# Performance work log

Hardware: AMD Instinct MI355X
Metric: run time of the kernel (lower is better)

The kernel has to match this reference:

```python
import jax, jax.numpy as jnp
import numpy as np

B, L, D, H = 1, 1024, 768, 12
h = D // H  # 64
EPS = 1e-5
ALPHA = 0.01  # leaky relu slope


def setup_inputs() -> dict:
    key = jax.random.key(0)
    ks = jax.random.split(key, 10)
    s = 0.02
    f32 = jnp.float32
    return {
        "x": jax.random.normal(ks[0], (B, L, D), f32),
        "filters": jax.random.normal(ks[1], (L, h), f32) * s,  # spectral filters [L, h]
        "wq_w": jax.random.normal(ks[2], (D, D), f32) * s,
        "wq_b": jnp.zeros((D,), f32),
        "wk_w": jax.random.normal(ks[3], (D, D), f32) * s,
        "wk_b": jnp.zeros((D,), f32),
        "wv_w": jax.random.normal(ks[4], (D, D), f32) * s,
        "wv_b": jnp.zeros((D,), f32),
        "wo_w": jax.random.normal(ks[5], (D, D), f32) * s,
        "wo_b": jnp.zeros((D,), f32),
        "wg_w": jax.random.normal(ks[6], (h * h, 1), f32) * s,
        "wg_b": jnp.zeros((1,), f32),
        "qk_scale": jnp.ones((1, H, 1), f32) + jax.random.normal(ks[7], (1, H, 1), f32) * 0.02,
        "kv_scale": jnp.ones((1, H, 1, 1, 1), f32) + jax.random.normal(ks[8], (1, H, 1, 1, 1), f32) * 0.02,
    }


def _causal_fft_conv(f, u):
    """Per-head-channel causal FFT convolution. f: [L,h], u: [B,H,L,h] -> [B,H,L,h]."""
    n = 2 * L  # >= L + L - 1 for linear (full) convolution
    Ff = jnp.fft.rfft(f, n=n, axis=0)            # [n//2+1, h]
    Uf = jnp.fft.rfft(u, n=n, axis=2)            # [B,H,n//2+1,h]
    y = jnp.fft.irfft(Uf * Ff[None, None], n=n, axis=2)
    return y[:, :, :L, :]


def _l2norm(t):
    # matches F.normalize(dim=-1): x / max(||x||, 1e-12)
    nrm = jnp.sqrt(jnp.sum(t * t, axis=-1, keepdims=True))
    return t / jnp.maximum(nrm, 1e-12)


def _combine(a, b):
    """Associative combine: (m, s, n, Z, g) running-max / exp-sum / exp-weighted-v / outer-product / gate-sum."""
    m_x, s_x, n_x, Z_x, g_x = a
    m_y, s_y, n_y, Z_y, g_y = b
    m = jnp.maximum(m_x, m_y)
    ex = jnp.exp(m_x - m)
    ey = jnp.exp(m_y - m)
    return (m,
            s_x * ex + s_y * ey,
            n_x * ex[..., None] + n_y * ey[..., None],
            Z_x + Z_y,
            g_x + g_y)


def reference(x, filters, wq_w, wq_b, wk_w, wk_b, wv_w, wv_b, wo_w, wo_b,
              wg_w, wg_b, qk_scale, kv_scale):
    # split heads: [B,H,L,h]
    bhld = x.reshape(B, L, H, h).transpose(0, 2, 1, 3)
    # spectral filtering (tensordot_conv): per-channel causal conv with filters
    xt = _causal_fft_conv(filters, bhld)                       # [B,H,L,h]
    xt = xt.transpose(0, 2, 1, 3).reshape(B, L, D)             # [B,L,D]

    q = (xt @ wq_w + wq_b).reshape(B, L, H, h).transpose(0, 2, 1, 3)
    k = (xt @ wk_w + wk_b).reshape(B, L, H, h).transpose(0, 2, 1, 3)
    v = (xt @ wv_w + wv_b).reshape(B, L, H, h).transpose(0, 2, 1, 3)
    q, k, v = _l2norm(q), _l2norm(k), _l2norm(v)

    sim = jnp.einsum('bhld,bhld->bhl', q, k) * qk_scale         # [B,H,L]
    # Z[b,h,s,p,n] = v[b,h,s,p] * k[b,h,s,n]
    Z = jnp.einsum('bhsn,bhsp->bhspn', k, v) * kv_scale         # [B,H,L,h,h]

    gate_logits = Z.reshape(B, H, L, h * h) @ wg_w + wg_b       # [B,H,L,1]
    gl = jnp.where(gate_logits > 0, gate_logits, ALPHA * gate_logits)
    gates = (gl * gl + EPS)[..., 0]                             # [B,H,L]
    gated_Z = Z * gates[..., None, None]

    leaves = (sim, jnp.ones_like(sim), v, gated_Z, gates)
    m_s, s_s, n_s, Z_s, g_s = jax.lax.associative_scan(_combine, leaves, axis=2)

    linear_attn = n_s / (s_s[..., None] + EPS)                  # [B,H,L,h]
    softmax_w = jnp.exp(sim - m_s) / (s_s + EPS)                # [B,H,L]
    Hm = Z_s / (g_s[..., None, None] + EPS)                     # [B,H,L,h,h]
    ctx = jnp.einsum('bhtp,bhtpn->bhtn', q, Hm)                 # [B,H,L,h]
    qla = linear_attn
    lerp = ctx + (qla - ctx) * softmax_w[..., None]

    y = lerp.transpose(0, 2, 1, 3).reshape(B, L, D)
    return y @ wo_w + wo_b
```

## Files before the change

### kernel.cpp

```cpp
#include <hip/hip_runtime.h>
#include <hip/hip_bf16.h>

constexpr int LS = 1024;
constexpr int DM = 768;
constexpr int NH = 12;
constexpr int HD = 64;
constexpr float EPSF = 1e-5f;
constexpr float ALPHAF = 0.01f;

constexpr int SG = 16;
constexpr int NTL = LS / SG;
constexpr int WSZ = DM * DM;
constexpr int NPAR = 8;

typedef unsigned short u16;
typedef __attribute__((ext_vector_type(8))) short bf16x8;
typedef __attribute__((ext_vector_type(8))) unsigned short u16x8;
typedef __attribute__((ext_vector_type(4))) float f32x4;

__device__ __forceinline__ u16 f2b(float f) {
  unsigned u = __float_as_uint(f);
  u += 0x7FFFu + ((u >> 16) & 1u);
  return (u16)(u >> 16);
}
__device__ __forceinline__ float b2f(u16 b) {
  return __uint_as_float((unsigned)b << 16);
}

__device__ __forceinline__ void gld16(const u16* g, void* l) {
  __builtin_amdgcn_global_load_lds(
      (const __attribute__((address_space(1))) void*)g,
      (__attribute__((address_space(3))) void*)l, 16, 0, 0);
}

__global__ __launch_bounds__(256) void conv_txw_kernel(
    const float* __restrict__ x, const float* __restrict__ f,
    const float* __restrict__ wq, const float* __restrict__ wk,
    const float* __restrict__ wv, const float* __restrict__ wo,
    u16* __restrict__ wT, u16* __restrict__ pbase) {
  extern __shared__ char smem[];
  const int b = blockIdx.x;
  const int tid = threadIdx.x;

  if (b >= 1536) {
    const int b2 = b - 1536;
    const int kb = (b2 % 12) * 64, nb = ((b2 / 12) % 12) * 64, z = b2 / 144;
    const float* src = (z == 0) ? wq : (z == 1) ? wk : (z == 2) ? wv : wo;
    u16* dst = wT + (size_t)z * WSZ;
    float (*T)[65] = (float(*)[65])smem;
#pragma unroll
    for (int rep = 0; rep < 4; ++rep) {
      const int r = rep * 16 + (tid >> 4);
      const int c4 = (tid & 15) * 4;
      const float4 v4 = *(const float4*)(src + (size_t)(kb + r) * DM + nb + c4);
      T[r][c4] = v4.x; T[r][c4 + 1] = v4.y; T[r][c4 + 2] = v4.z; T[r][c4 + 3] = v4.w;
    }
    __syncthreads();
#pragma unroll
    for (int rep = 0; rep < 4; ++rep) {
      const int n = rep * 16 + (tid >> 4);
      const int k4 = (tid & 15) * 4;
      ushort4 o;
      o.x = f2b(T[k4 + 0][n]); o.y = f2b(T[k4 + 1][n]);
      o.z = f2b(T[k4 + 2][n]); o.w = f2b(T[k4 + 3][n]);
      *(ushort4*)(dst + (size_t)(nb + n) * DM + kb + k4) = o;
    }
    return;
  }

  const int i    = b & 15;
  const int head = (b >> 4) % 12;
  const int par  = b / 192;
  const int c    = tid & 63;
  const int sg   = tid >> 6;
  const int tbase = i * 64;
  const int l0w   = tbase + sg * 16;
  u16* __restrict__ xt_p = pbase + (size_t)par * LS * DM;

  float4 (*Xs2)[64] = (float4(*)[64])smem;

  {
    const float4 z4 = make_float4(0.f, 0.f, 0.f, 0.f);
#pragma unroll
    for (int k = 0; k < 3; ++k) {
      const int lin = k * 256 + tid;
      const int g   = lin >> 6;
      const int cc  = lin & 63;
      const int grp = (g < 4) ? g : (16 + g);
      Xs2[grp][cc] = z4;
    }
  }

  float acc[16];
#pragma unroll
  for (int t = 0; t < 16; ++t) acc[t] = 0.f;

  const float* xg   = x + head * HD + c;
  const float* fcol = f + c;

  for (int j = par; j <= i; j += NPAR) {
    const int sbase = j * 64;
    const int b0 = (j < i) ? (tbase - sbase - 64) : 0;
#pragma unroll
    for (int k = 0; k < 4; ++k) {
      const int m  = sg + 4 * k;
      const int ss = 4 * m;
      float4 v4;
      v4.x = xg[(sbase + ss + 0) * DM];
      v4.y = xg[(sbase + ss + 1) * DM];
      v4.z = xg[(sbase + ss + 2) * DM];
      v4.w = xg[(sbase + ss + 3) * DM];
      Xs2[4 + m][c] = v4;
    }
    __syncthreads();

    const int dstart = (j < i) ? (b0 + sg * 16) : 0;
    const int nsteps = (j < i) ? 5 : (sg + 1);
    for (int k = 0; k < nsteps; ++k) {
      const int d0    = dstart + 16 * k;
      const int rbase = l0w - d0 - sbase;
      float fr[16];
#pragma unroll
      for (int m = 0; m < 16; ++m) fr[m] = fcol[(d0 + m) * HD];
      float xw[32];
      const int xgb = rbase >> 2;
#pragma unroll
      for (int m = 0; m < 8; ++m) {
        const float4 v4 = Xs2[xgb + m][c];
        xw[4 * m + 0] = v4.x; xw[4 * m + 1] = v4.y;
        xw[4 * m + 2] = v4.z; xw[4 * m + 3] = v4.w;
      }
#pragma unroll
      for (int li = 0; li < 16; ++li)
#pragma unroll
        for (int dd = 0; dd < 16; ++dd)
          acc[li] = fmaf(fr[dd], xw[li - dd + 16], acc[li]);
    }
    __syncthreads();
  }

#pragma unroll
  for (int li = 0; li < 16; ++li)
    xt_p[(size_t)(l0w + li) * DM + head * HD + c] = f2b(acc[li]);
}

__global__ __launch_bounds__(256) void pack_xt(const u16* __restrict__ pbase,
                                               u16* __restrict__ xtb) {
  const size_t NT = (size_t)LS * DM;
  const size_t i = ((size_t)blockIdx.x * 256 + threadIdx.x) * 8;
  float s[8] = {};
#pragma unroll
  for (int p = 0; p < NPAR; ++p) {
    const u16x8 v8 = *(const u16x8*)(pbase + p * NT + i);
#pragma unroll
    for (int e = 0; e < 8; ++e) s[e] += b2f(v8[e]);
  }
  u16x8 o;
#pragma unroll
  for (int e = 0; e < 8; ++e) o[e] = f2b(s[e]);
  *(u16x8*)(xtb + i) = o;
}

__global__ __launch_bounds__(256) void qkv_mfma(const u16* __restrict__ xtb,
                                                const u16* __restrict__ wT,
                                                const float* __restrict__ bq,
                                                const float* __restrict__ bk,
                                                const float* __restrict__ bv,
                                                float* __restrict__ qo,
                                                float* __restrict__ ko,
                                                float* __restrict__ vo) {
  const int b = blockIdx.x;
  const int xcd = b & 7, j = b >> 3;
  const int unit = xcd * 9 + (j >> 3), sub = j & 7;
  const int z = unit / 24, rem = unit % 24;
  const int ct = rem >> 1, rt = (rem & 1) * 8 + sub;

  __shared__ u16 As[64 * 64];
  __shared__ u16 Bs[64 * 64];

  const int tid = threadIdx.x, w = tid >> 6, l = tid & 63;
  const int wr = w >> 1, wc = w & 1;

  const int srow1 = tid >> 3, sc16 = tid & 7;
  const int c16L1 = sc16 ^ (srow1 & 7);
  const int srow2 = srow1 + 32;
  const int c16L2 = sc16 ^ (srow2 & 7);

  const u16* wz = wT + (size_t)z * WSZ;
  const u16* Ag1 = xtb + (size_t)(rt * 64 + srow1) * DM + c16L1 * 8;
  const u16* Ag2 = xtb + (size_t)(rt * 64 + srow2) * DM + c16L2 * 8;
  const u16* Bg1 = wz + (size_t)(ct * 64 + srow1) * DM + c16L1 * 8;
  const u16* Bg2 = wz + (size_t)(ct * 64 + srow2) * DM + c16L2 * 8;

  char* lA = (char*)As + w * 1024;
  char* lB = (char*)Bs + w * 1024;

  f32x4 acc[2][2] = {};
  for (int kb = 0; kb < DM; kb += 64) {
    gld16(Ag1 + kb, lA);
    gld16(Ag2 + kb, lA + 4096);
    gld16(Bg1 + kb, lB);
    gld16(Bg2 + kb, lB + 4096);
    __syncthreads();
#pragma unroll
    for (int kk = 0; kk < 2; ++kk) {
      bf16x8 a[2], bb[2];
#pragma unroll
      for (int ar = 0; ar < 2; ++ar) {
        const int row = wr * 32 + ar * 16 + (l & 15);
        const int c16 = ((kk << 2) + (l >> 4)) ^ (row & 7);
        a[ar] = *(const bf16x8*)((char*)As + row * 128 + c16 * 16);
      }
#pragma unroll
      for (int bc = 0; bc < 2; ++bc) {
        const int col = wc * 32 + bc * 16 + (l & 15);
        const int c16 = ((kk << 2) + (l >> 4)) ^ (col & 7);
        bb[bc] = *(const bf16x8*)((char*)Bs + col * 128 + c16 * 16);
      }
#pragma unroll
      for (int ar = 0; ar < 2; ++ar)
#pragma unroll
        for (int bc = 0; bc < 2; ++bc)
          acc[ar][bc] = __builtin_amdgcn_mfma_f32_16x16x32_bf16(
              a[ar], bb[bc], acc[ar][bc], 0, 0, 0);
    }
    __syncthreads();
  }

  const float* bias = (z == 0) ? bq : (z == 1) ? bk : bv;
  float* out = (z == 0) ? qo : (z == 1) ? ko : vo;
  const int rbase = rt * 64 + wr * 32 + ((l >> 4) << 2);
  const int cb = wc * 32 + (l & 15);
#pragma unroll
  for (int ar = 0; ar < 2; ++ar)
#pragma unroll
    for (int bc = 0; bc < 2; ++bc) {
      const int col = cb + bc * 16;
      const float bbv = bias[ct * 64 + col];
#pragma unroll
      for (int r = 0; r < 4; ++r)
        out[((size_t)ct * LS + rbase + ar * 16 + r) * HD + col] =
            acc[ar][bc][r] + bbv;
    }
}

__global__ __launch_bounds__(256) void out_mfma(const u16* __restrict__ lerpb,
                                                const u16* __restrict__ woT,
                                                const float* __restrict__ bias,
                                                float* __restrict__ out) {
  const int b = blockIdx.x;
  const int xcd = b & 7, j = b >> 3;
  const int unit = xcd * 3 + (j >> 3), sub = j & 7;
  const int ct = unit >> 1, rt = (unit & 1) * 8 + sub;

  __shared__ u16 As[64 * 64];
  __shared__ u16 Bs[64 * 64];

  const int tid = threadIdx.x, w = tid >> 6, l = tid & 63;
  const int wr = w >> 1, wc = w & 1;

  const int srow1 = tid >> 3, sc16 = tid & 7;
  const int c16L1 = sc16 ^ (srow1 & 7);
  const int srow2 = srow1 + 32;
  const int c16L2 = sc16 ^ (srow2 & 7);

  const u16* Ag1 = lerpb + (size_t)(rt * 64 + srow1) * DM + c16L1 * 8;
  const u16* Ag2 = lerpb + (size_t)(rt * 64 + srow2) * DM + c16L2 * 8;
  const u16* Bg1 = woT + (size_t)(ct * 64 + srow1) * DM + c16L1 * 8;
  const u16* Bg2 = woT + (size_t)(ct * 64 + srow2) * DM + c16L2 * 8;

  char* lA = (char*)As + w * 1024;
  char* lB = (char*)Bs + w * 1024;

  f32x4 acc[2][2] = {};
  for (int kb = 0; kb < DM; kb += 64) {
    gld16(Ag1 + kb, lA);
    gld16(Ag2 + kb, lA + 4096);
    gld16(Bg1 + kb, lB);
    gld16(Bg2 + kb, lB + 4096);
    __syncthreads();
#pragma unroll
    for (int kk = 0; kk < 2; ++kk) {
      bf16x8 a[2], bb[2];
#pragma unroll
      for (int ar = 0; ar < 2; ++ar) {
        const int row = wr * 32 + ar * 16 + (l & 15);
        const int c16 = ((kk << 2) + (l >> 4)) ^ (row & 7);
        a[ar] = *(const bf16x8*)((char*)As + row * 128 + c16 * 16);
      }
#pragma unroll
      for (int bc = 0; bc < 2; ++bc) {
        const int col = wc * 32 + bc * 16 + (l & 15);
        const int c16 = ((kk << 2) + (l >> 4)) ^ (col & 7);
        bb[bc] = *(const bf16x8*)((char*)Bs + col * 128 + c16 * 16);
      }
#pragma unroll
      for (int ar = 0; ar < 2; ++ar)
#pragma unroll
        for (int bc = 0; bc < 2; ++bc)
          acc[ar][bc] = __builtin_amdgcn_mfma_f32_16x16x32_bf16(
              a[ar], bb[bc], acc[ar][bc], 0, 0, 0);
    }
    __syncthreads();
  }

  const int rbase = rt * 64 + wr * 32 + ((l >> 4) << 2);
  const int cb = wc * 32 + (l & 15);
#pragma unroll
  for (int ar = 0; ar < 2; ++ar)
#pragma unroll
    for (int bc = 0; bc < 2; ++bc) {
      const int col = ct * 64 + cb + bc * 16;
      const float bbv = bias[col];
#pragma unroll
      for (int r = 0; r < 4; ++r)
        out[(size_t)(rbase + ar * 16 + r) * DM + col] = acc[ar][bc][r] + bbv;
    }
}

__global__ __launch_bounds__(256) void nsg_state_kernel(
    float* __restrict__ q, float* __restrict__ k, float* __restrict__ v,
    const float* __restrict__ wg, const float* __restrict__ wgb,
    const float* __restrict__ qk_scale, const float* __restrict__ kv_scale,
    float* __restrict__ sim, float* __restrict__ gates,
    float* __restrict__ states, float* __restrict__ nes) {
  const int j = blockIdx.x, head = blockIdx.y;
  const int s0 = j * SG;
  const int tid = threadIdx.x;
  const int wid = tid >> 6, lane = tid & 63;
  __shared__ alignas(16) float Vs[SG][68];
  __shared__ alignas(16) float Kg[SG][68];
  __shared__ float Es[SG];

  auto red = [](float x) {
#pragma unroll
    for (int o = 32; o; o >>= 1) x += __shfl_xor(x, o);
    return x;
  };

  const float qks = qk_scale[head], kvs = kv_scale[head], wb = wgb[0];
#pragma unroll
  for (int it = 0; it < 4; ++it) {
    const int rr = wid * 4 + it;
    const size_t idx = ((size_t)head * LS + s0 + rr) * HD + lane;
    float qv = q[idx], kv = k[idx], vv = v[idx];
    const float qn = fmaxf(sqrtf(red(qv * qv)), 1e-12f);
    const float kn = fmaxf(sqrtf(red(kv * kv)), 1e-12f);
    const float vn = fmaxf(sqrtf(red(vv * vv)), 1e-12f);
    qv /= qn; kv /= kn; vv /= vn;
    q[idx] = qv; k[idx] = kv; v[idx] = vv;
    const float s = red(qv * kv) * qks;
    Vs[rr][lane] = vv;
    float t = 0.f;
#pragma unroll 8
    for (int p = 0; p < 64; ++p) t = fmaf(Vs[rr][p], wg[p * 64 + lane], t);
    float gl = red(t * kv) * kvs + wb;
    gl = gl > 0.f ? gl : ALPHAF * gl;
    const float g = gl * gl + EPSF;
    Kg[rr][lane] = kv * g;
    if (lane == 0) {
      sim[head * LS + s0 + rr] = s;
      gates[head * LS + s0 + rr] = g;
      Es[rr] = expf(s);
    }
  }
  __syncthreads();

  const int p0 = (tid >> 4) * 4, n0 = (tid & 15) * 4;
  float acc[4][4] = {};
  for (int s = 0; s < SG; ++s) {
    const float4 ra = *(const float4*)&Vs[s][p0];
    const float4 rb = *(const float4*)&Kg[s][n0];
    const float av[4] = {ra.x, ra.y, ra.z, ra.w};
    const float bv[4] = {rb.x, rb.y, rb.z, rb.w};
#pragma unroll
    for (int i = 0; i < 4; ++i)
#pragma unroll
      for (int jj = 0; jj < 4; ++jj)
        acc[i][jj] = fmaf(av[i], bv[jj], acc[i][jj]);
  }
  float* Sout = states + (size_t)(head * NTL + j) * 4096;
#pragma unroll
  for (int i = 0; i < 4; ++i)
    *(float4*)&Sout[(p0 + i) * 64 + n0] =
        make_float4(acc[i][0], acc[i][1], acc[i][2], acc[i][3]);

  if (tid < HD) {
    float ne = 0.f;
#pragma unroll
    for (int s = 0; s < SG; ++s) ne = fmaf(Es[s], Vs[s][tid], ne);
    nes[(size_t)(head * NTL + j) * HD + tid] = ne;
  }
}

__global__ __launch_bounds__(1024) void scan_prefix_kernel(
    const float* __restrict__ sim, const float* __restrict__ gates,
    float* __restrict__ m_s, float* __restrict__ Sraw, float* __restrict__ g_s,
    float* __restrict__ states, float* __restrict__ nes) {
  const int head = blockIdx.x;
  const int tid = threadIdx.x, lane = tid & 63, wid = tid >> 6;
  __shared__ float wm[16], wS[16], wg2[16];

  const float sv = sim[head * LS + tid];
  float m = sv, S = expf(sv), g = gates[head * LS + tid];
#pragma unroll
  for (int off = 1; off < 64; off <<= 1) {
    const float pm = __shfl_up(m, off);
    const float pS = __shfl_up(S, off);
    const float pg = __shfl_up(g, off);
    if (lane >= off) { m = fmaxf(m, pm); S += pS; g += pg; }
  }
  if (lane == 63) { wm[wid] = m; wS[wid] = S; wg2[wid] = g; }
  __syncthreads();
  for (int w2 = 0; w2 < wid; ++w2) {
    m = fmaxf(m, wm[w2]); S += wS[w2]; g += wg2[w2];
  }
  m_s[head * LS + tid] = m;
  Sraw[head * LS + tid] = S;
  g_s[head * LS + tid] = g;

  {
    float4 acc = make_float4(0.f, 0.f, 0.f, 0.f);
    float* base = states + (size_t)head * NTL * 4096 + tid * 4;
#pragma unroll 4
    for (int jj = 0; jj < NTL; ++jj) {
      float4* p = (float4*)(base + (size_t)jj * 4096);
      const float4 s4 = *p;
      *p = acc;
      acc.x += s4.x; acc.y += s4.y; acc.z += s4.z; acc.w += s4.w;
    }
  }
  if (tid < HD) {
    float a = 0.f;
    float* nb = nes + (size_t)head * NTL * HD + tid;
#pragma unroll 4
    for (int jj = 0; jj < NTL; ++jj) {
      float* p = nb + (size_t)jj * HD;
      const float t = *p;
      *p = a;
      a += t;
    }
  }
}

__global__ __launch_bounds__(256) void apply_kernel(const float* __restrict__ q,
                                                    const float* __restrict__ k,
                                                    const float* __restrict__ v,
                                                    const float* __restrict__ sim,
                                                    const float* __restrict__ gates,
                                                    const float* __restrict__ m_s,
                                                    const float* __restrict__ Sraw,
                                                    const float* __restrict__ g_s,
                                                    const float* __restrict__ states,
                                                    const float* __restrict__ nes,
                                                    const float* __restrict__ kv_scale,
                                                    u16* __restrict__ lerpb) {
  const int bt = blockIdx.x, head = blockIdx.y;
  const int t0 = bt * SG;
  const int tid = threadIdx.x;
  __shared__ alignas(16) float Ps[64][68];
  __shared__ alignas(16) float Qs[SG][68];
  __shared__ alignas(16) float Vs[SG][68];
  __shared__ alignas(16) float Ks[SG][68];
  __shared__ alignas(16) float NEp[64];
  __shared__ float Ag[SG][SG + 1];
  __shared__ float Es[SG], Gs[SG];

  const float* Pg = states + (size_t)(head * NTL + bt) * 4096;
#pragma unroll
  for (int rep = 0; rep < 4; ++rep) {
    const int lin = rep * 1024 + tid * 4;
    *(float4*)&Ps[lin >> 6][lin & 63] = *(const float4*)(Pg + lin);
  }
  {
    const int r = tid >> 4, c = (tid & 15) * 4;
    const size_t rowbase = ((size_t)head * LS + t0 + r) * HD;
    *(float4*)&Qs[r][c] = *(const float4*)(q + rowbase + c);
    *(float4*)&Ks[r][c] = *(const float4*)(k + rowbase + c);
    *(float4*)&Vs[r][c] = *(const float4*)(v + rowbase + c);
  }
  if (tid < SG) {
    Es[tid] = expf(sim[head * LS + t0 + tid]);
    Gs[tid] = gates[head * LS + t0 + tid];
  }
  if (tid < HD) NEp[tid] = nes[(size_t)(head * NTL + bt) * HD + tid];
  __syncthreads();

  {
    const int t = tid >> 4, s = tid & 15;
    float a = 0.f;
    if (s <= t) {
#pragma unroll
      for (int p = 0; p < 64; p += 4) {
        const float4 q4 = *(const float4*)&Qs[t][p];
        const float4 v4 = *(const float4*)&Vs[s][p];
        a = fmaf(q4.x, v4.x, a); a = fmaf(q4.y, v4.y, a);
        a = fmaf(q4.z, v4.z, a); a = fmaf(q4.w, v4.w, a);
      }
      a *= Gs[s];
    }
    Ag[t][s] = a;
  }
  __syncthreads();

  const int r = tid >> 4, c0 = (tid & 15) * 4;
  float4 O = make_float4(0.f, 0.f, 0.f, 0.f);
#pragma unroll 8
  for (int p = 0; p < 64; ++p) {
    const float qv = Qs[r][p];
    const float4 p4 = *(const float4*)&Ps[p][c0];
    O.x = fmaf(qv, p4.x, O.x); O.y = fmaf(qv, p4.y, O.y);
    O.z = fmaf(qv, p4.z, O.z); O.w = fmaf(qv, p4.w, O.w);
  }
  float4 Nn = *(const float4*)&NEp[c0];
  for (int s = 0; s <= r; ++s) {
    const float ag = Ag[r][s];
    const float es = Es[s];
    const float4 k4 = *(const float4*)&Ks[s][c0];
    const float4 v4 = *(const float4*)&Vs[s][c0];
    O.x = fmaf(ag, k4.x, O.x); O.y = fmaf(ag, k4.y, O.y);
    O.z = fmaf(ag, k4.z, O.z); O.w = fmaf(ag, k4.w, O.w);
    Nn.x = fmaf(es, v4.x, Nn.x); Nn.y = fmaf(es, v4.y, Nn.y);
    Nn.z = fmaf(es, v4.z, Nn.z); Nn.w = fmaf(es, v4.w, Nn.w);
  }

  const int t = t0 + r;
  const float m  = m_s[head * LS + t];
  const float em = expf(-m);
  const float ss = Sraw[head * LS + t] * em;
  const float inv = 1.f / (ss + EPSF);
  const float sw  = expf(sim[head * LS + t] - m) * inv;
  const float gi  = kv_scale[head] / (g_s[head * LS + t] + EPSF);
  const float ei  = em * inv;
  float rx, ry, rz, rw;
  { const float cx = O.x * gi, la = Nn.x * ei; rx = cx + (la - cx) * sw; }
  { const float cx = O.y * gi, la = Nn.y * ei; ry = cx + (la - cx) * sw; }
  { const float cx = O.z * gi, la = Nn.z * ei; rz = cx + (la - cx) * sw; }
  { const float cx = O.w * gi, la = Nn.w * ei; rw = cx + (la - cx) * sw; }
  ushort4 ob;
  ob.x = f2b(rx); ob.y = f2b(ry); ob.z = f2b(rz); ob.w = f2b(rw);
  *(ushort4*)&lerpb[(size_t)t * DM + head * HD + c0] = ob;
}

extern "C" void kernel_launch(void* const* d_in, const int* in_sizes, int n_in,
                              void* d_out, int out_size, void* d_ws, size_t ws_size,
                              hipStream_t stream) {
  (void)in_sizes; (void)n_in; (void)out_size; (void)ws_size;
  const float* x        = (const float*)d_in[0];
  const float* filters  = (const float*)d_in[1];
  const float* wq_w     = (const float*)d_in[2];
  const float* wq_b     = (const float*)d_in[3];
  const float* wk_w     = (const float*)d_in[4];
  const float* wk_b     = (const float*)d_in[5];
  const float* wv_w     = (const float*)d_in[6];
  const float* wv_b     = (const float*)d_in[7];
  const float* wo_w     = (const float*)d_in[8];
  const float* wo_b     = (const float*)d_in[9];
  const float* wg_w     = (const float*)d_in[10];
  const float* wg_b     = (const float*)d_in[11];
  const float* qk_scale = (const float*)d_in[12];
  const float* kv_scale = (const float*)d_in[13];

  float* ws = (float*)d_ws;
  const size_t NT = (size_t)LS * DM;
  float* q     = ws;
  float* k     = ws + NT;
  float* v     = ws + 2 * NT;
  float* sim   = ws + 3 * NT;
  float* gates = sim + NH * LS;
  float* m_s   = gates + NH * LS;
  float* Sraw  = m_s + NH * LS;
  float* g_s   = Sraw + NH * LS;
  float* states = g_s + NH * LS;
  float* nes    = states + (size_t)NH * NTL * 4096;
  u16*   xtb    = (u16*)(nes + (size_t)NH * NTL * HD);
  u16*   wT     = xtb + NT;
  u16*   lerpb  = wT + 4 * (size_t)WSZ;
  u16*   pbase  = lerpb + NT;

  conv_txw_kernel<<<dim3(2112), 256, 28672, stream>>>(
      x, filters, wq_w, wk_w, wv_w, wo_w, wT, pbase);
  pack_xt<<<dim3(NT / 2048), 256, 0, stream>>>(pbase, xtb);
  qkv_mfma<<<dim3(576), 256, 0, stream>>>(xtb, wT, wq_b, wk_b, wv_b, q, k, v);
  nsg_state_kernel<<<dim3(NTL, NH), 256, 0, stream>>>(
      q, k, v, wg_w, wg_b, qk_scale, kv_scale, sim, gates, states, nes);
  scan_prefix_kernel<<<dim3(NH), 1024, 0, stream>>>(
      sim, gates, m_s, Sraw, g_s, states, nes);
  apply_kernel<<<dim3(NTL, NH), 256, 0, stream>>>(
      q, k, v, sim, gates, m_s, Sraw, g_s, states, nes, kv_scale, lerpb);
  out_mfma<<<dim3(192), 256, 0, stream>>>(
      lerpb, wT + 3 * (size_t)WSZ, wo_b, (float*)d_out);
}
```

Before: 107.6 us.

## Fuse Q/K/V projections per tile and split state prefix scan across blocks

The QKV GEMM now has each block compute all three projections for one row/column tile, loading the shared A tile once and reusing it against three B tiles. The grid drops from 576 to 192 blocks and the block-to-XCD mapping is reorganised. Separately, the state prefix scan is split into four chunks per head, so 48 blocks share the 64-step sequential sweep instead of 12. The fusion trades fewer blocks, more registers (three accumulator sets) and more LDS for less redundant A loading.

```diff
diff --git a/kernel.cpp b/kernel.cpp
--- a/kernel.cpp
+++ b/kernel.cpp
@@ -171,12 +171,11 @@
                                                 float* __restrict__ vo) {
   const int b = blockIdx.x;
   const int xcd = b & 7, j = b >> 3;
-  const int unit = xcd * 9 + (j >> 3), sub = j & 7;
-  const int z = unit / 24, rem = unit % 24;
-  const int ct = rem >> 1, rt = (rem & 1) * 8 + sub;
+  const int rt = (xcd & 3) * 4 + j / 6;
+  const int ct = (xcd >> 2) * 6 + j % 6;
 
   __shared__ u16 As[64 * 64];
-  __shared__ u16 Bs[64 * 64];
+  __shared__ u16 Bs[3][64 * 64];
 
   const int tid = threadIdx.x, w = tid >> 6, l = tid & 63;
   const int wr = w >> 1, wc = w & 1;
@@ -186,25 +185,28 @@
   const int srow2 = srow1 + 32;
   const int c16L2 = sc16 ^ (srow2 & 7);
 
-  const u16* wz = wT + (size_t)z * WSZ;
   const u16* Ag1 = xtb + (size_t)(rt * 64 + srow1) * DM + c16L1 * 8;
   const u16* Ag2 = xtb + (size_t)(rt * 64 + srow2) * DM + c16L2 * 8;
-  const u16* Bg1 = wz + (size_t)(ct * 64 + srow1) * DM + c16L1 * 8;
-  const u16* Bg2 = wz + (size_t)(ct * 64 + srow2) * DM + c16L2 * 8;
 
   char* lA = (char*)As + w * 1024;
-  char* lB = (char*)Bs + w * 1024;
-
-  f32x4 acc[2][2] = {};
+
+  f32x4 acc[3][2][2] = {};
   for (int kb = 0; kb < DM; kb += 64) {
     gld16(Ag1 + kb, lA);
     gld16(Ag2 + kb, lA + 4096);
-    gld16(Bg1 + kb, lB);
-    gld16(Bg2 + kb, lB + 4096);
+#pragma unroll
+    for (int z = 0; z < 3; ++z) {
+      const u16* wz = wT + (size_t)z * WSZ;
+      const u16* Bg1 = wz + (size_t)(ct * 64 + srow1) * DM + c16L1 * 8;
+      const u16* Bg2 = wz + (size_t)(ct * 64 + srow2) * DM + c16L2 * 8;
+      char* lB = (char*)Bs[z] + w * 1024;
+      gld16(Bg1 + kb, lB);
+      gld16(Bg2 + kb, lB + 4096);
+    }
     __syncthreads();
 #pragma unroll
     for (int kk = 0; kk < 2; ++kk) {
-      bf16x8 a[2], bb[2];
+      bf16x8 a[2];
 #pragma unroll
       for (int ar = 0; ar < 2; ++ar) {
         const int row = wr * 32 + ar * 16 + (l & 15);
@@ -212,36 +214,45 @@
         a[ar] = *(const bf16x8*)((char*)As + row * 128 + c16 * 16);
       }
 #pragma unroll
-      for (int bc = 0; bc < 2; ++bc) {
-        const int col = wc * 32 + bc * 16 + (l & 15);
-        const int c16 = ((kk << 2) + (l >> 4)) ^ (col & 7);
-        bb[bc] = *(const bf16x8*)((char*)Bs + col * 128 + c16 * 16);
-      }
-#pragma unroll
-      for (int ar = 0; ar < 2; ++ar)
-#pragma unroll
-        for (int bc = 0; bc < 2; ++bc)
-          acc[ar][bc] = __builtin_amdgcn_mfma_f32_16x16x32_bf16(
-              a[ar], bb[bc], acc[ar][bc], 0, 0, 0);
-    }
-    __syncthreads();
-  }
-
-  const float* bias = (z == 0) ? bq : (z == 1) ? bk : bv;
-  float* out = (z == 0) ? qo : (z == 1) ? ko : vo;
+      for (int z = 0; z < 3; ++z) {
+        bf16x8 bb[2];
+#pragma unroll
+        for (int bc = 0; bc < 2; ++bc) {
+          const int col = wc * 32 + bc * 16 + (l & 15);
+          const int c16 = ((kk << 2) + (l >> 4)) ^ (col & 7);
+          bb[bc] = *(const bf16x8*)((char*)Bs[z] + col * 128 + c16 * 16);
+        }
+#pragma unroll
+        for (int ar = 0; ar < 2; ++ar)
+#pragma unroll
+          for (int bc = 0; bc < 2; ++bc)
+            acc[z][ar][bc] = __builtin_amdgcn_mfma_f32_16x16x32_bf16(
+                a[ar], bb[bc], acc[z][ar][bc], 0, 0, 0);
+      }
+    }
+    __syncthreads();
+  }
+
+  const float* biasArr[3] = {bq, bk, bv};
+  float* outArr[3] = {qo, ko, vo};
   const int rbase = rt * 64 + wr * 32 + ((l >> 4) << 2);
   const int cb = wc * 32 + (l & 15);
 #pragma unroll
-  for (int ar = 0; ar < 2; ++ar)
-#pragma unroll
-    for (int bc = 0; bc < 2; ++bc) {
-      const int col = cb + bc * 16;
-      const float bbv = bias[ct * 64 + col];
-#pragma unroll
-      for (int r = 0; r < 4; ++r)
-        out[((size_t)ct * LS + rbase + ar * 16 + r) * HD + col] =
-            acc[ar][bc][r] + bbv;
-    }
+  for (int z = 0; z < 3; ++z) {
+    const float* bias = biasArr[z];
+    float* out = outArr[z];
+#pragma unroll
+    for (int ar = 0; ar < 2; ++ar)
+#pragma unroll
+      for (int bc = 0; bc < 2; ++bc) {
+        const int col = cb + bc * 16;
+        const float bbv = bias[ct * 64 + col];
+#pragma unroll
+        for (int r = 0; r < 4; ++r)
+          out[((size_t)ct * LS + rbase + ar * 16 + r) * HD + col] =
+              acc[z][ar][bc][r] + bbv;
+      }
+  }
 }
 
 __global__ __launch_bounds__(256) void out_mfma(const u16* __restrict__ lerpb,
@@ -397,45 +408,48 @@
     const float* __restrict__ sim, const float* __restrict__ gates,
     float* __restrict__ m_s, float* __restrict__ Sraw, float* __restrict__ g_s,
     float* __restrict__ states, float* __restrict__ nes) {
-  const int head = blockIdx.x;
+  const int head = blockIdx.x, chunk = blockIdx.y;
   const int tid = threadIdx.x, lane = tid & 63, wid = tid >> 6;
-  __shared__ float wm[16], wS[16], wg2[16];
-
-  const float sv = sim[head * LS + tid];
-  float m = sv, S = expf(sv), g = gates[head * LS + tid];
-#pragma unroll
-  for (int off = 1; off < 64; off <<= 1) {
-    const float pm = __shfl_up(m, off);
-    const float pS = __shfl_up(S, off);
-    const float pg = __shfl_up(g, off);
-    if (lane >= off) { m = fmaxf(m, pm); S += pS; g += pg; }
-  }
-  if (lane == 63) { wm[wid] = m; wS[wid] = S; wg2[wid] = g; }
-  __syncthreads();
-  for (int w2 = 0; w2 < wid; ++w2) {
-    m = fmaxf(m, wm[w2]); S += wS[w2]; g += wg2[w2];
-  }
-  m_s[head * LS + tid] = m;
-  Sraw[head * LS + tid] = S;
-  g_s[head * LS + tid] = g;
+
+  if (chunk == 0) {
+    __shared__ float wm[16], wS[16], wg2[16];
+    const float sv = sim[head * LS + tid];
+    float m = sv, S = expf(sv), g = gates[head * LS + tid];
+#pragma unroll
+    for (int off = 1; off < 64; off <<= 1) {
+      const float pm = __shfl_up(m, off);
+      const float pS = __shfl_up(S, off);
+      const float pg = __shfl_up(g, off);
+      if (lane >= off) { m = fmaxf(m, pm); S += pS; g += pg; }
+    }
+    if (lane == 63) { wm[wid] = m; wS[wid] = S; wg2[wid] = g; }
+    __syncthreads();
+    for (int w2 = 0; w2 < wid; ++w2) {
+      m = fmaxf(m, wm[w2]); S += wS[w2]; g += wg2[w2];
+    }
+    m_s[head * LS + tid] = m;
+    Sraw[head * LS + tid] = S;
+    g_s[head * LS + tid] = g;
+
+    if (tid < HD) {
+      float a = 0.f;
+      float* nb = nes + (size_t)head * NTL * HD + tid;
+#pragma unroll 4
+      for (int jj = 0; jj < NTL; ++jj) {
+        float* p = nb + (size_t)jj * HD;
+        const float t = *p;
+        *p = a;
+        a += t;
+      }
+    }
+  }
 
   {
-    float4 acc = make_float4(0.f, 0.f, 0.f, 0.f);
-    float* base = states + (size_t)head * NTL * 4096 + tid * 4;
+    float a = 0.f;
+    float* base = states + (size_t)head * NTL * 4096 + chunk * 1024 + tid;
 #pragma unroll 4
     for (int jj = 0; jj < NTL; ++jj) {
-      float4* p = (float4*)(base + (size_t)jj * 4096);
-      const float4 s4 = *p;
-      *p = acc;
-      acc.x += s4.x; acc.y += s4.y; acc.z += s4.z; acc.w += s4.w;
-    }
-  }
-  if (tid < HD) {
-    float a = 0.f;
-    float* nb = nes + (size_t)head * NTL * HD + tid;
-#pragma unroll 4
-    for (int jj = 0; jj < NTL; ++jj) {
-      float* p = nb + (size_t)jj * HD;
+      float* p = base + (size_t)jj * 4096;
       const float t = *p;
       *p = a;
       a += t;
@@ -581,10 +595,10 @@
   conv_txw_kernel<<<dim3(2112), 256, 28672, stream>>>(
       x, filters, wq_w, wk_w, wv_w, wo_w, wT, pbase);
   pack_xt<<<dim3(NT / 2048), 256, 0, stream>>>(pbase, xtb);
-  qkv_mfma<<<dim3(576), 256, 0, stream>>>(xtb, wT, wq_b, wk_b, wv_b, q, k, v);
+  qkv_mfma<<<dim3(192), 256, 0, stream>>>(xtb, wT, wq_b, wk_b, wv_b, q, k, v);
   nsg_state_kernel<<<dim3(NTL, NH), 256, 0, stream>>>(
       q, k, v, wg_w, wg_b, qk_scale, kv_scale, sim, gates, states, nes);
-  scan_prefix_kernel<<<dim3(NH), 1024, 0, stream>>>(
+  scan_prefix_kernel<<<dim3(NH, 4), 1024, 0, stream>>>(
       sim, gates, m_s, Sraw, g_s, states, nes);
   apply_kernel<<<dim3(NTL, NH), 256, 0, stream>>>(
       q, k, v, sim, gates, m_s, Sraw, g_s, states, nes, kv_scale, lerpb);
```

Result: faster. 101.5 us (median of 3 runs) (-5.7%).
